# Kernel optimization log

Measured on AMD Instinct MI355X. Metric: run time of the kernel, lower is better.

The kernel has to match this reference:

```python
import jax, jax.numpy as jnp
import numpy as np

E, K, D = 50000, 8, 256
NH = 4
HD = D // NH
SCALE = HD ** -0.5
EPS = 1e-8


def setup_inputs() -> dict:
    key = jax.random.key(0)
    ks = jax.random.split(key, 16)
    p = lambda k, shp: (jax.random.normal(k, shp, dtype=jnp.float32) * 0.02)
    return {
        "x_i": jax.random.normal(ks[0], (E, D), dtype=jnp.float32),
        "x_j": jax.random.normal(ks[1], (E, D), dtype=jnp.float32),
        "h_seq_i": jax.random.normal(ks[2], (E, K, D), dtype=jnp.float32),
        "h_seq_j": jax.random.normal(ks[3], (E, K, D), dtype=jnp.float32),
        "edge_emb": jax.random.normal(ks[4], (E, D), dtype=jnp.float32),
        "Wq": p(ks[5], (D, D)), "bq": jnp.zeros((D,), jnp.float32),
        "Wk": p(ks[6], (D, D)), "bk": jnp.zeros((D,), jnp.float32),
        "We1": p(ks[7], (D, D // 2)), "be1": jnp.zeros((D // 2,), jnp.float32),
        "We2": p(ks[8], (D // 2, 1)), "be2": jnp.zeros((1,), jnp.float32),
        "Wo1": p(ks[9], (3, 16)), "bo1": jnp.zeros((16,), jnp.float32),
        "Wo2": p(ks[10], (16, 1)), "bo2": jnp.zeros((1,), jnp.float32),
    }


def reference(x_i, x_j, h_seq_i, h_seq_j, edge_emb,
              Wq, bq, Wk, bk, We1, be1, We2, be2, Wo1, bo1, Wo2, bo2):
    # (A) attribute alignment: cosine similarity mapped to (0,1)
    num = jnp.sum(x_i * x_j, axis=-1)
    den = jnp.maximum(jnp.linalg.norm(x_i, axis=-1), EPS) * \
          jnp.maximum(jnp.linalg.norm(x_j, axis=-1), EPS)
    attr_score = (num / den + 1.0) / 2.0  # [E]

    # (B) activity alignment: tiny cross-attention, mean of softmax diagonal
    Q = (jnp.einsum('ekd,df->ekf', h_seq_i, Wq) + bq).reshape(E, K, NH, HD)
    Kv = (jnp.einsum('ekd,df->ekf', h_seq_j, Wk) + bk).reshape(E, K, NH, HD)
    scores = jnp.einsum('eqhd,ekhd->ehqk', Q, Kv) * SCALE  # [E,NH,K,K]
    attn = jax.nn.softmax(scores, axis=-1)
    diag = jnp.diagonal(attn, axis1=-2, axis2=-1)  # [E,NH,K]
    activity_score = diag.mean(axis=(-1, -2))  # [E]

    # (C) edge plausibility MLP (exact GELU as in torch default)
    h = jax.nn.gelu(edge_emb @ We1 + be1, approximate=False)
    edge_score = jax.nn.sigmoid((h @ We2 + be2)[..., 0])  # [E]

    signals = jnp.stack([attr_score, activity_score, edge_score], axis=-1)  # [E,3]
    out = jax.nn.gelu(signals @ Wo1 + bo1, approximate=False) @ Wo2 + bo2
    return jax.nn.sigmoid(out[..., 0])  # [E]
```

## Files before the change

### kernel.cpp

```cpp
#include <hip/hip_runtime.h>

#define E_TOT   50000
#define DD      256
#define TE      4
#define NGROUP  (E_TOT / TE)
#define SCALE_V 0.125f

typedef __attribute__((ext_vector_type(4))) float f32x4;
typedef __attribute__((ext_vector_type(8))) short short8;

__device__ __forceinline__ unsigned short f2bf(float f) {
    unsigned u = __float_as_uint(f);
    u += 0x7fffu + ((u >> 16) & 1u);
    return (unsigned short)(u >> 16);
}
__device__ __forceinline__ float gelu_exact(float x) {
    return 0.5f * x * (1.0f + erff(x * 0.70710678118654752440f));
}
__device__ __forceinline__ float sigmoidf(float x) {
    return 1.0f / (1.0f + __expf(-x));
}

__device__ __forceinline__ void dma_row16(const float* gbase, float* lds) {
    const int lane = threadIdx.x & 63;
    auto gp = (const __attribute__((address_space(1))) char*)(gbase) + lane * 16;
    auto lp = (__attribute__((address_space(3))) char*)(lds);
    __builtin_amdgcn_global_load_lds(gp, lp, 16, 0, 0);
}

__global__ void prep_weights(const float* __restrict__ Wq,
                             const float* __restrict__ Wk,
                             const float* __restrict__ We1,
                             unsigned short* __restrict__ wqT,
                             unsigned short* __restrict__ wkT,
                             unsigned short* __restrict__ w1T) {
    int i = blockIdx.x * 256 + threadIdx.x;
    if (i < 65536) {
        int k = i >> 8, n = i & 255;
        wqT[n * 256 + k] = f2bf(Wq[i]);
    } else if (i < 131072) {
        int j = i - 65536;
        int k = j >> 8, n = j & 255;
        wkT[n * 256 + k] = f2bf(Wk[j]);
    } else {
        int j = i - 131072;
        int k = j >> 7, n = j & 127;
        w1T[n * 256 + k] = f2bf(We1[j]);
    }
}

__device__ __forceinline__ void proj_gemm(const unsigned short (*A)[260],
                                          const unsigned short* __restrict__ Wt,
                                          f32x4 acc[2][4], int lr, int lq, int w) {
    #pragma unroll
    for (int ks = 0; ks < 8; ++ks) {
        short8 a0 = *(const short8*)&A[lr][ks * 32 + lq * 8];
        short8 a1 = *(const short8*)&A[16 + lr][ks * 32 + lq * 8];
        #pragma unroll
        for (int n = 0; n < 4; ++n) {
            const int col = (w * 4 + n) * 16 + lr;
            short8 bv = *(const short8*)(Wt + col * 256 + ks * 32 + lq * 8);
            acc[0][n] = __builtin_amdgcn_mfma_f32_16x16x32_bf16(a0, bv, acc[0][n], 0, 0, 0);
            acc[1][n] = __builtin_amdgcn_mfma_f32_16x16x32_bf16(a1, bv, acc[1][n], 0, 0, 0);
        }
    }
}

__device__ __forceinline__ void writeback(unsigned short (*T)[260],
                                          const f32x4 acc[2][4],
                                          const float* __restrict__ bias,
                                          int lr, int lq, int w) {
    #pragma unroll
    for (int n = 0; n < 4; ++n) {
        const int col = (w * 4 + n) * 16 + lr;
        const float bs = bias[col];
        #pragma unroll
        for (int m = 0; m < 2; ++m) {
            #pragma unroll
            for (int v = 0; v < 4; ++v) {
                const int row = m * 16 + lq * 4 + v;
                T[row][col] = f2bf(acc[m][n][v] + bs);
            }
        }
    }
}

__global__ __launch_bounds__(256, 3)
void fused_all(const float* __restrict__ x_i,
               const float* __restrict__ x_j,
               const float* __restrict__ h_i,
               const float* __restrict__ h_j,
               const float* __restrict__ emb,
               const unsigned short* __restrict__ wqT,
               const unsigned short* __restrict__ wkT,
               const unsigned short* __restrict__ w1T,
               const float* __restrict__ bq,
               const float* __restrict__ bk,
               const float* __restrict__ be1,
               const float* __restrict__ We2,
               const float* __restrict__ be2,
               const float* __restrict__ Wo1,
               const float* __restrict__ bo1,
               const float* __restrict__ Wo2,
               const float* __restrict__ bo2,
               float* __restrict__ out) {
    __shared__ __align__(16) unsigned char ldsA[33280];
    __shared__ __align__(16) unsigned char ldsH[16640];
    __shared__ float sEdgeP[4][4];

    float* bufA32 = (float*)ldsA;
    unsigned short (*bufHI)[260] = (unsigned short (*)[260])ldsH;
    unsigned short (*tQ)[260]    = (unsigned short (*)[260])ldsA;
    unsigned short (*tK)[260]    = (unsigned short (*)[260])(ldsA + 16640);

    const int t  = threadIdx.x;
    const int w  = t >> 6;
    const int l  = t & 63;
    const int lr = l & 15, lq = l >> 4;
    const int g  = blockIdx.x;
    const size_t rowbase = (size_t)g * 32;

    #pragma unroll
    for (int rr = 0; rr < 8; ++rr) {
        const int r = w * 8 + rr;
        dma_row16(h_i + (rowbase + r) * DD, bufA32 + r * DD);
    }
    const int e = g * TE + w;
    float attr;
    {
        f32x4 a = *(const f32x4*)(x_i + (size_t)e * DD + l * 4);
        f32x4 b = *(const f32x4*)(x_j + (size_t)e * DD + l * 4);
        float dot = a[0]*b[0] + a[1]*b[1] + a[2]*b[2] + a[3]*b[3];
        float ni  = a[0]*a[0] + a[1]*a[1] + a[2]*a[2] + a[3]*a[3];
        float nj  = b[0]*b[0] + b[1]*b[1] + b[2]*b[2] + b[3]*b[3];
        #pragma unroll
        for (int off = 1; off < 64; off <<= 1) {
            dot += __shfl_xor(dot, off);
            ni  += __shfl_xor(ni,  off);
            nj  += __shfl_xor(nj,  off);
        }
        attr = (dot / (fmaxf(sqrtf(ni), 1e-8f) * fmaxf(sqrtf(nj), 1e-8f)) + 1.0f) * 0.5f;
    }
    __syncthreads();

    f32x4 stg[8];
    #pragma unroll
    for (int i = 0; i < 8; ++i) stg[i] = *(const f32x4*)(bufA32 + (i * 256 + t) * 4);
    __syncthreads();

    #pragma unroll
    for (int rr = 0; rr < 8; ++rr) {
        const int r = w * 8 + rr;
        dma_row16(h_j + (rowbase + r) * DD, bufA32 + r * DD);
    }
    #pragma unroll
    for (int i = 0; i < 8; ++i) {
        const int f = i * 256 + t, r = f >> 6, u = f & 63;
        *(ushort4*)&bufHI[r][u * 4] = make_ushort4(f2bf(stg[i][0]), f2bf(stg[i][1]),
                                                   f2bf(stg[i][2]), f2bf(stg[i][3]));
    }
    __syncthreads();

    f32x4 accQ[2][4] = {};
    proj_gemm(bufHI, wqT, accQ, lr, lq, w);
    f32x4 accE[2] = {};
    {
        const float* embrow = emb + ((size_t)g * TE + (lr & 3)) * DD;
        #pragma unroll
        for (int ks = 0; ks < 8; ++ks) {
            f32x4 e0 = *(const f32x4*)(embrow + ks * 32 + lq * 8);
            f32x4 e1 = *(const f32x4*)(embrow + ks * 32 + lq * 8 + 4);
            short8 ae;
            ae[0] = (short)f2bf(e0[0]); ae[1] = (short)f2bf(e0[1]);
            ae[2] = (short)f2bf(e0[2]); ae[3] = (short)f2bf(e0[3]);
            ae[4] = (short)f2bf(e1[0]); ae[5] = (short)f2bf(e1[1]);
            ae[6] = (short)f2bf(e1[2]); ae[7] = (short)f2bf(e1[3]);
            #pragma unroll
            for (int n = 0; n < 2; ++n) {
                const int col = w * 32 + n * 16 + lr;
                short8 bv = *(const short8*)(w1T + col * 256 + ks * 32 + lq * 8);
                accE[n] = __builtin_amdgcn_mfma_f32_16x16x32_bf16(ae, bv, accE[n], 0, 0, 0);
            }
        }
    }
    #pragma unroll
    for (int i = 0; i < 8; ++i) stg[i] = *(const f32x4*)(bufA32 + (i * 256 + t) * 4);
    __syncthreads();

    #pragma unroll
    for (int i = 0; i < 8; ++i) {
        const int f = i * 256 + t, r = f >> 6, u = f & 63;
        *(ushort4*)&bufHI[r][u * 4] = make_ushort4(f2bf(stg[i][0]), f2bf(stg[i][1]),
                                                   f2bf(stg[i][2]), f2bf(stg[i][3]));
    }
    writeback(tQ, accQ, bq, lr, lq, w);
    __syncthreads();

    f32x4 accK[2][4] = {};
    proj_gemm(bufHI, wkT, accK, lr, lq, w);
    __syncthreads();

    writeback(tK, accK, bk, lr, lq, w);
    {
        float p[4] = {0.f, 0.f, 0.f, 0.f};
        #pragma unroll
        for (int n = 0; n < 2; ++n) {
            const int col = w * 32 + n * 16 + lr;
            const float b1 = be1[col], w2 = We2[col];
            #pragma unroll
            for (int v = 0; v < 4; ++v)
                p[v] += gelu_exact(accE[n][v] + b1) * w2;
        }
        #pragma unroll
        for (int off = 1; off < 16; off <<= 1) {
            #pragma unroll
            for (int v = 0; v < 4; ++v) p[v] += __shfl_xor(p[v], off);
        }
        if (l == 0) {
            sEdgeP[w][0] = p[0]; sEdgeP[w][1] = p[1];
            sEdgeP[w][2] = p[2]; sEdgeP[w][3] = p[3];
        }
    }
    __syncthreads();

    float contrib = 0.f;
    #pragma unroll
    for (int h = 0; h < 4; ++h) {
        f32x4 s = {};
        #pragma unroll
        for (int ks = 0; ks < 2; ++ks) {
            short8 qa = *(const short8*)&tQ[w * 8 + (lr & 7)][h * 64 + ks * 32 + lq * 8];
            short8 kb = *(const short8*)&tK[w * 8 + (lr & 7)][h * 64 + ks * 32 + lq * 8];
            s = __builtin_amdgcn_mfma_f32_16x16x32_bf16(qa, kb, s, 0, 0, 0);
        }
        #pragma unroll
        for (int v = 0; v < 4; ++v) {
            float sc = s[v] * SCALE_V;
            float m = sc;
            m = fmaxf(m, __shfl_xor(m, 1));
            m = fmaxf(m, __shfl_xor(m, 2));
            m = fmaxf(m, __shfl_xor(m, 4));
            float pe = __expf(sc - m);
            float sum = pe;
            sum += __shfl_xor(sum, 1);
            sum += __shfl_xor(sum, 2);
            sum += __shfl_xor(sum, 4);
            if (lq < 2 && lr == lq * 4 + v) contrib += pe / sum;
        }
    }
    #pragma unroll
    for (int off = 1; off < 64; off <<= 1) contrib += __shfl_xor(contrib, off);
    const float act = contrib * (1.0f / 32.0f);

    const float es = sigmoidf(sEdgeP[0][w] + sEdgeP[1][w] + sEdgeP[2][w] +
                              sEdgeP[3][w] + be2[0]);
    float r = 0.f;
    if (l < 16) {
        float z = attr * Wo1[l] + act * Wo1[16 + l] + es * Wo1[32 + l] + bo1[l];
        r = gelu_exact(z) * Wo2[l];
    }
    r += __shfl_xor(r, 1);
    r += __shfl_xor(r, 2);
    r += __shfl_xor(r, 4);
    r += __shfl_xor(r, 8);
    if (l == 0) out[e] = sigmoidf(r + bo2[0]);
}

extern "C" void kernel_launch(void* const* d_in, const int* in_sizes, int n_in,
                              void* d_out, int out_size, void* d_ws, size_t ws_size,
                              hipStream_t stream) {
    const float* x_i  = (const float*)d_in[0];
    const float* x_j  = (const float*)d_in[1];
    const float* h_i  = (const float*)d_in[2];
    const float* h_j  = (const float*)d_in[3];
    const float* emb  = (const float*)d_in[4];
    const float* Wq   = (const float*)d_in[5];
    const float* bq   = (const float*)d_in[6];
    const float* Wk   = (const float*)d_in[7];
    const float* bk   = (const float*)d_in[8];
    const float* We1  = (const float*)d_in[9];
    const float* be1  = (const float*)d_in[10];
    const float* We2  = (const float*)d_in[11];
    const float* be2  = (const float*)d_in[12];
    const float* Wo1  = (const float*)d_in[13];
    const float* bo1  = (const float*)d_in[14];
    const float* Wo2  = (const float*)d_in[15];
    const float* bo2  = (const float*)d_in[16];
    float* out = (float*)d_out;

    unsigned short* wqT = (unsigned short*)d_ws;
    unsigned short* wkT = wqT + 65536;
    unsigned short* w1T = wkT + 65536;

    prep_weights<<<640, 256, 0, stream>>>(Wq, Wk, We1, wqT, wkT, w1T);
    fused_all<<<NGROUP, 256, 0, stream>>>(x_i, x_j, h_i, h_j, emb,
                                          wqT, wkT, w1T,
                                          bq, bk, be1, We2, be2,
                                          Wo1, bo1, Wo2, bo2, out);
}
```

Baseline: 636.1 us.

## Load both h sequences into registers upfront and reuse LDS buffers in place

Instead of staging h_i and then h_j through an fp32 LDS buffer with global_load_lds, each thread issues register loads for both sequences together, converts them to bf16, and writes them into two bf16 LDS tiles. The Q and K projections run back to back, and their results overwrite the input tiles in place. The softmax is reorganised to use per-lane max and sum plus a single cross-quarter shuffle, and the cosine reduction is merged into the final reduction loop. Together these cut the barrier count and shrink LDS enough to request occupancy 4, at the cost of 64 extra VGPRs holding in-flight loads.

```diff
diff --git a/kernel.cpp b/kernel.cpp
--- a/kernel.cpp
+++ b/kernel.cpp
@@ -19,13 +19,6 @@
 }
 __device__ __forceinline__ float sigmoidf(float x) {
     return 1.0f / (1.0f + __expf(-x));
-}
-
-__device__ __forceinline__ void dma_row16(const float* gbase, float* lds) {
-    const int lane = threadIdx.x & 63;
-    auto gp = (const __attribute__((address_space(1))) char*)(gbase) + lane * 16;
-    auto lp = (__attribute__((address_space(3))) char*)(lds);
-    __builtin_amdgcn_global_load_lds(gp, lp, 16, 0, 0);
 }
 
 __global__ void prep_weights(const float* __restrict__ Wq,
@@ -85,7 +78,7 @@
     }
 }
 
-__global__ __launch_bounds__(256, 3)
+__global__ __launch_bounds__(256, 4)
 void fused_all(const float* __restrict__ x_i,
                const float* __restrict__ x_j,
                const float* __restrict__ h_i,
@@ -104,67 +97,48 @@
                const float* __restrict__ Wo2,
                const float* __restrict__ bo2,
                float* __restrict__ out) {
-    __shared__ __align__(16) unsigned char ldsA[33280];
-    __shared__ __align__(16) unsigned char ldsH[16640];
+    __shared__ unsigned short bufHI[32][260];
+    __shared__ unsigned short bufHJ[32][260];
     __shared__ float sEdgeP[4][4];
-
-    float* bufA32 = (float*)ldsA;
-    unsigned short (*bufHI)[260] = (unsigned short (*)[260])ldsH;
-    unsigned short (*tQ)[260]    = (unsigned short (*)[260])ldsA;
-    unsigned short (*tK)[260]    = (unsigned short (*)[260])(ldsA + 16640);
 
     const int t  = threadIdx.x;
     const int w  = t >> 6;
     const int l  = t & 63;
     const int lr = l & 15, lq = l >> 4;
     const int g  = blockIdx.x;
-    const size_t rowbase = (size_t)g * 32;
-
-    #pragma unroll
-    for (int rr = 0; rr < 8; ++rr) {
-        const int r = w * 8 + rr;
-        dma_row16(h_i + (rowbase + r) * DD, bufA32 + r * DD);
-    }
-    const int e = g * TE + w;
-    float attr;
+    const int e  = g * TE + w;
+    const size_t hbase = (size_t)g * (TE * 8 * DD);
+
+    f32x4 xa = *(const f32x4*)(x_i + (size_t)e * DD + l * 4);
+    f32x4 xb = *(const f32x4*)(x_j + (size_t)e * DD + l * 4);
+    f32x4 si[8], sj[8];
+    #pragma unroll
+    for (int i = 0; i < 8; ++i)
+        si[i] = *(const f32x4*)(h_i + hbase + (size_t)(i * 256 + t) * 4);
+    #pragma unroll
+    for (int i = 0; i < 8; ++i)
+        sj[i] = *(const f32x4*)(h_j + hbase + (size_t)(i * 256 + t) * 4);
+    __builtin_amdgcn_sched_barrier(0);
+
+    #pragma unroll
+    for (int i = 0; i < 8; ++i) {
+        const int f = i * 256 + t;
+        *(ushort4*)&bufHI[f >> 6][(f & 63) * 4] =
+            make_ushort4(f2bf(si[i][0]), f2bf(si[i][1]), f2bf(si[i][2]), f2bf(si[i][3]));
+    }
+    #pragma unroll
+    for (int i = 0; i < 8; ++i) {
+        const int f = i * 256 + t;
+        *(ushort4*)&bufHJ[f >> 6][(f & 63) * 4] =
+            make_ushort4(f2bf(sj[i][0]), f2bf(sj[i][1]), f2bf(sj[i][2]), f2bf(sj[i][3]));
+    }
+    float cd = xa[0]*xb[0] + xa[1]*xb[1] + xa[2]*xb[2] + xa[3]*xb[3];
+    float ci = xa[0]*xa[0] + xa[1]*xa[1] + xa[2]*xa[2] + xa[3]*xa[3];
+    float cj = xb[0]*xb[0] + xb[1]*xb[1] + xb[2]*xb[2] + xb[3]*xb[3];
+    __syncthreads();
+
     {
-        f32x4 a = *(const f32x4*)(x_i + (size_t)e * DD + l * 4);
-        f32x4 b = *(const f32x4*)(x_j + (size_t)e * DD + l * 4);
-        float dot = a[0]*b[0] + a[1]*b[1] + a[2]*b[2] + a[3]*b[3];
-        float ni  = a[0]*a[0] + a[1]*a[1] + a[2]*a[2] + a[3]*a[3];
-        float nj  = b[0]*b[0] + b[1]*b[1] + b[2]*b[2] + b[3]*b[3];
-        #pragma unroll
-        for (int off = 1; off < 64; off <<= 1) {
-            dot += __shfl_xor(dot, off);
-            ni  += __shfl_xor(ni,  off);
-            nj  += __shfl_xor(nj,  off);
-        }
-        attr = (dot / (fmaxf(sqrtf(ni), 1e-8f) * fmaxf(sqrtf(nj), 1e-8f)) + 1.0f) * 0.5f;
-    }
-    __syncthreads();
-
-    f32x4 stg[8];
-    #pragma unroll
-    for (int i = 0; i < 8; ++i) stg[i] = *(const f32x4*)(bufA32 + (i * 256 + t) * 4);
-    __syncthreads();
-
-    #pragma unroll
-    for (int rr = 0; rr < 8; ++rr) {
-        const int r = w * 8 + rr;
-        dma_row16(h_j + (rowbase + r) * DD, bufA32 + r * DD);
-    }
-    #pragma unroll
-    for (int i = 0; i < 8; ++i) {
-        const int f = i * 256 + t, r = f >> 6, u = f & 63;
-        *(ushort4*)&bufHI[r][u * 4] = make_ushort4(f2bf(stg[i][0]), f2bf(stg[i][1]),
-                                                   f2bf(stg[i][2]), f2bf(stg[i][3]));
-    }
-    __syncthreads();
-
-    f32x4 accQ[2][4] = {};
-    proj_gemm(bufHI, wqT, accQ, lr, lq, w);
-    f32x4 accE[2] = {};
-    {
+        f32x4 accE[2] = {};
         const float* embrow = emb + ((size_t)g * TE + (lr & 3)) * DD;
         #pragma unroll
         for (int ks = 0; ks < 8; ++ks) {
@@ -182,26 +156,6 @@
                 accE[n] = __builtin_amdgcn_mfma_f32_16x16x32_bf16(ae, bv, accE[n], 0, 0, 0);
             }
         }
-    }
-    #pragma unroll
-    for (int i = 0; i < 8; ++i) stg[i] = *(const f32x4*)(bufA32 + (i * 256 + t) * 4);
-    __syncthreads();
-
-    #pragma unroll
-    for (int i = 0; i < 8; ++i) {
-        const int f = i * 256 + t, r = f >> 6, u = f & 63;
-        *(ushort4*)&bufHI[r][u * 4] = make_ushort4(f2bf(stg[i][0]), f2bf(stg[i][1]),
-                                                   f2bf(stg[i][2]), f2bf(stg[i][3]));
-    }
-    writeback(tQ, accQ, bq, lr, lq, w);
-    __syncthreads();
-
-    f32x4 accK[2][4] = {};
-    proj_gemm(bufHI, wkT, accK, lr, lq, w);
-    __syncthreads();
-
-    writeback(tK, accK, bk, lr, lq, w);
-    {
         float p[4] = {0.f, 0.f, 0.f, 0.f};
         #pragma unroll
         for (int n = 0; n < 2; ++n) {
@@ -221,6 +175,14 @@
             sEdgeP[w][2] = p[2]; sEdgeP[w][3] = p[3];
         }
     }
+
+    f32x4 accQ[2][4] = {};
+    f32x4 accK[2][4] = {};
+    proj_gemm(bufHI, wqT, accQ, lr, lq, w);
+    proj_gemm(bufHJ, wkT, accK, lr, lq, w);
+    __syncthreads();
+    writeback(bufHI, accQ, bq, lr, lq, w);
+    writeback(bufHJ, accK, bk, lr, lq, w);
     __syncthreads();
 
     float contrib = 0.f;
@@ -229,31 +191,39 @@
         f32x4 s = {};
         #pragma unroll
         for (int ks = 0; ks < 2; ++ks) {
-            short8 qa = *(const short8*)&tQ[w * 8 + (lr & 7)][h * 64 + ks * 32 + lq * 8];
-            short8 kb = *(const short8*)&tK[w * 8 + (lr & 7)][h * 64 + ks * 32 + lq * 8];
-            s = __builtin_amdgcn_mfma_f32_16x16x32_bf16(qa, kb, s, 0, 0, 0);
-        }
-        #pragma unroll
-        for (int v = 0; v < 4; ++v) {
-            float sc = s[v] * SCALE_V;
-            float m = sc;
-            m = fmaxf(m, __shfl_xor(m, 1));
-            m = fmaxf(m, __shfl_xor(m, 2));
-            m = fmaxf(m, __shfl_xor(m, 4));
-            float pe = __expf(sc - m);
-            float sum = pe;
-            sum += __shfl_xor(sum, 1);
-            sum += __shfl_xor(sum, 2);
-            sum += __shfl_xor(sum, 4);
-            if (lq < 2 && lr == lq * 4 + v) contrib += pe / sum;
-        }
-    }
-    #pragma unroll
-    for (int off = 1; off < 64; off <<= 1) contrib += __shfl_xor(contrib, off);
-    const float act = contrib * (1.0f / 32.0f);
-
+            short8 a = *(const short8*)&bufHJ[w * 8 + (lr & 7)][h * 64 + ks * 32 + lq * 8];
+            short8 b = *(const short8*)&bufHI[w * 8 + (lr & 7)][h * 64 + ks * 32 + lq * 8];
+            s = __builtin_amdgcn_mfma_f32_16x16x32_bf16(a, b, s, 0, 0, 0);
+        }
+        float sc[4];
+        #pragma unroll
+        for (int v = 0; v < 4; ++v) sc[v] = s[v] * SCALE_V;
+        float m4 = fmaxf(fmaxf(sc[0], sc[1]), fmaxf(sc[2], sc[3]));
+        float mx = fmaxf(m4, __shfl_xor(m4, 16));
+        float pe[4], ps = 0.f;
+        #pragma unroll
+        for (int v = 0; v < 4; ++v) { pe[v] = __expf(sc[v] - mx); ps += pe[v]; }
+        float tot = ps + __shfl_xor(ps, 16);
+        float pd = 0.f;
+        #pragma unroll
+        for (int v = 0; v < 4; ++v)
+            pd = (((lq * 4 + v) & 7) == (lr & 7)) ? pe[v] : pd;
+        if (lr < 8 && lq < 2) contrib += pd / tot;
+    }
+
+    #pragma unroll
+    for (int off = 1; off < 64; off <<= 1) {
+        contrib += __shfl_xor(contrib, off);
+        cd += __shfl_xor(cd, off);
+        ci += __shfl_xor(ci, off);
+        cj += __shfl_xor(cj, off);
+    }
+    const float act  = contrib * (1.0f / 32.0f);
+    const float attr = (cd / (fmaxf(sqrtf(ci), 1e-8f) * fmaxf(sqrtf(cj), 1e-8f))
+                        + 1.0f) * 0.5f;
     const float es = sigmoidf(sEdgeP[0][w] + sEdgeP[1][w] + sEdgeP[2][w] +
                               sEdgeP[3][w] + be2[0]);
+
     float r = 0.f;
     if (l < 16) {
         float z = attr * Wo1[l] + act * Wo1[16 + l] + es * Wo1[32 + l] + bo1[l];
```

Measured after the change: 655.7 us. +3.1%, slower.
